# Optimization experiments

Measured on AMD Instinct MI355X. Metric: run time of the kernel, lower is better.

## Reference

```python
import jax, jax.numpy as jnp
import numpy as np

EPS = 1e-5
AVG_D_LOG = 2.302585092994046  # avg_d['log'] = log(10)

N, D, F, FE = 65536, 16, 64, 16
POST_IN = (4 * 3 + 1) * F  # (n_agg*n_scalers + 1) * in_dim = 832


def setup_inputs() -> dict:
    key = jax.random.key(0)
    ks = jax.random.split(key, 8)
    h = jax.random.normal(ks[0], (N, F), dtype=jnp.float32)
    edge_attr = jax.random.normal(ks[1], (N, D, FE), dtype=jnp.float32)
    nbr_idx = jax.random.randint(ks[2], (N, D), 0, N)
    pre_in = 2 * F + FE
    W_pre = jax.random.normal(ks[3], (pre_in, F), dtype=jnp.float32) / np.sqrt(pre_in)
    b_pre = jnp.zeros((F,), dtype=jnp.float32)
    W_post1 = jax.random.normal(ks[4], (POST_IN, F), dtype=jnp.float32) / np.sqrt(POST_IN)
    b_post1 = jnp.zeros((F,), dtype=jnp.float32)
    W_post2 = jax.random.normal(ks[5], (F, F), dtype=jnp.float32) / np.sqrt(F)
    b_post2 = jnp.zeros((F,), dtype=jnp.float32)
    return {"h": h, "edge_attr": edge_attr, "nbr_idx": nbr_idx,
            "W_pre": W_pre, "b_pre": b_pre,
            "W_post1": W_post1, "b_post1": b_post1,
            "W_post2": W_post2, "b_post2": b_post2}


def reference(h, edge_attr, nbr_idx, W_pre, b_pre, W_post1, b_post1, W_post2, b_post2):
    # pretrans: message MLP on cat([src_feat, dst_feat, edge_attr])
    h_src = h[nbr_idx]                                   # [N, D, F]
    h_dst = jnp.broadcast_to(h[:, None, :], h_src.shape)  # [N, D, F]
    z = jnp.concatenate([h_src, h_dst, edge_attr], axis=-1)  # [N, D, 2F+FE]
    e = jax.nn.relu(jnp.einsum('ndi,io->ndo', z, W_pre) + b_pre)  # [N, D, F]

    # multi-aggregator neighbor reduction (dim=-2)
    mean = jnp.mean(e, axis=-2)
    mx = jnp.max(e, axis=-2)
    mn = jnp.min(e, axis=-2)
    var = jax.nn.relu(jnp.mean(e * e, axis=-2) - mean * mean)
    std = jnp.sqrt(var + EPS)
    agg = jnp.concatenate([mean, mx, mn, std], axis=-1)  # [N, 4F]

    # degree scalers (fixed in-degree D)
    logD = jnp.asarray(np.log(D + 1.0), dtype=h.dtype)
    amp = agg * (logD / AVG_D_LOG)
    att = agg * (AVG_D_LOG / logD)
    agg = jnp.concatenate([agg, amp, att], axis=-1)      # [N, 12F]

    # posttrans MLP on cat([h, aggregated]) with residual (in_dim == out_dim)
    x = jnp.concatenate([h, agg], axis=-1)               # [N, 13F]
    x = jax.nn.relu(x @ W_post1 + b_post1)
    x = x @ W_post2 + b_post2
    return x + h
```

## Files before the change

### kernel.cpp

```cpp
#include <hip/hip_runtime.h>
#include <hip/hip_bf16.h>
#include <math.h>


#define N_NODES 65536
#define NBLK (N_NODES / 16)
#define GRID_PREP (NBLK + 64)
#define ASTRIDE 348
#define YSTRIDE 76

typedef float f32x4 __attribute__((ext_vector_type(4)));
typedef float f32x16 __attribute__((ext_vector_type(16)));
typedef short s16x8 __attribute__((ext_vector_type(8)));
typedef unsigned short us4 __attribute__((ext_vector_type(4)));
typedef int i32x4 __attribute__((ext_vector_type(4)));

__device__ __forceinline__ unsigned short f2bf(float f) {
    union { float f; unsigned int u; } v; v.f = f;
    unsigned int r = v.u + 0x7fffu + ((v.u >> 16) & 1u);
    return (unsigned short)(r >> 16);
}
__device__ __forceinline__ unsigned short f2bfh(float f) {
    __hip_bfloat16 b = __float2bfloat16(f);
    union { __hip_bfloat16 b; unsigned short u; } v; v.b = b; return v.u;
}
__device__ __forceinline__ float bf2f(unsigned short u) {
    union { unsigned int u; float f; } v; v.u = ((unsigned int)u) << 16; return v.f;
}
__device__ __forceinline__ unsigned char enc_u8(float x) {
    int q = __float2int_rn(x * 16.f) + 128;
    q = q < 0 ? 0 : (q > 255 ? 255 : q);
    return (unsigned char)q;
}

__global__ __launch_bounds__(256) void k_prep(const float* __restrict__ h,
                                              const float* __restrict__ Wpre,
                                              const float* __restrict__ b_pre,
                                              const float* __restrict__ Wp1,
                                              const float* __restrict__ Wp2,
                                              unsigned char* __restrict__ u8,
                                              unsigned short* __restrict__ vbf,
                                              unsigned short* __restrict__ wfullT,
                                              unsigned short* __restrict__ w3T,
                                              unsigned short* __restrict__ wp2T,
                                              float c1, float c2) {
    int t = threadIdx.x;
    if (blockIdx.x >= NBLK) {
        int c = blockIdx.x - NBLK;
        for (int k = t; k < 320; k += 256) {
            float v;
            if (k < 64) v = Wp1[k * 64 + c];
            else {
                int kk = k - 64;
                v = Wp1[(64 + kk) * 64 + c] + c1 * Wp1[(320 + kk) * 64 + c]
                                            + c2 * Wp1[(576 + kk) * 64 + c];
            }
            wfullT[c * 320 + k] = f2bf(v);
        }
        if (t < 16)              w3T[c * 16 + t]         = f2bf(Wpre[(128 + t) * 64 + c]);
        if (t >= 64 && t < 128)  wp2T[c * 64 + (t - 64)] = f2bf(Wp2[(t - 64) * 64 + c]);
        return;
    }

    __shared__ unsigned short hl[16 * 68];
    int lane = t & 63;
    int wv = __builtin_amdgcn_readfirstlane(t) >> 6;
    int c = lane & 15, g = lane >> 4;
    int node0 = blockIdx.x * 16;
    {
        int r = t >> 4, q = t & 15;
        float4 hv = *((const float4*)(h + (size_t)node0 * 64) + t);
        us4 o;
        o.x = f2bfh(hv.x); o.y = f2bfh(hv.y); o.z = f2bfh(hv.z); o.w = f2bfh(hv.w);
        *(us4*)&hl[r * 68 + q * 4] = o;
    }
    s16x8 bf[2][2];
    int woff = (wv < 2) ? 0 : 64;
    #pragma unroll
    for (int i2 = 0; i2 < 2; ++i2) {
        int wcol = ((wv & 1) * 32) + i2 * 16 + c;
        #pragma unroll
        for (int ks = 0; ks < 2; ++ks) {
            #pragma unroll
            for (int j = 0; j < 8; ++j)
                bf[i2][ks][j] = (short)f2bfh(Wpre[(woff + ks * 32 + g * 8 + j) * 64 + wcol]);
        }
    }
    __syncthreads();
    f32x4 acc0 = {0.f, 0.f, 0.f, 0.f}, acc1 = {0.f, 0.f, 0.f, 0.f};
    #pragma unroll
    for (int ks = 0; ks < 2; ++ks) {
        s16x8 a = *(const s16x8*)&hl[c * 68 + ks * 32 + g * 8];
        acc0 = __builtin_amdgcn_mfma_f32_16x16x32_bf16(a, bf[0][ks], acc0, 0, 0, 0);
        acc1 = __builtin_amdgcn_mfma_f32_16x16x32_bf16(a, bf[1][ks], acc1, 0, 0, 0);
    }
    #pragma unroll
    for (int i2 = 0; i2 < 2; ++i2) {
        int dcol = ((wv & 1) * 32) + i2 * 16 + c;
        const f32x4& av = i2 ? acc1 : acc0;
        if (wv < 2) {
            float bp = b_pre[dcol];
            #pragma unroll
            for (int i = 0; i < 4; ++i) {
                int row = g * 4 + i;
                u8[(size_t)(node0 + row) * 64 + dcol] = enc_u8(av[i] + bp);
            }
        } else {
            #pragma unroll
            for (int i = 0; i < 4; ++i) {
                int row = g * 4 + i;
                vbf[(size_t)(node0 + row) * 64 + dcol] = f2bfh(av[i]);
            }
        }
    }
}

__global__ __launch_bounds__(256, 4) void k_main(
    const float* __restrict__ h,
    const float* __restrict__ edge_attr,
    const int* __restrict__ nbr_idx,
    const float* __restrict__ b_post1,
    const float* __restrict__ b_post2,
    const unsigned char* __restrict__ u8,
    const unsigned short* __restrict__ vbf,
    const unsigned short* __restrict__ wfullT,
    const unsigned short* __restrict__ w3T,
    const unsigned short* __restrict__ wp2T,
    float* __restrict__ out) {
    __shared__ i32x4 u_lds4[1024];
    __shared__ i32x4 v_lds4[128];
    __shared__ unsigned short A_lds[16 * ASTRIDE];
    __shared__ unsigned short y1_lds[16 * YSTRIDE];
    unsigned char* u_lds = (unsigned char*)u_lds4;
    unsigned short* v_lds = (unsigned short*)v_lds4;

    int t = threadIdx.x;
    int lane = t & 63;
    int wu2 = __builtin_amdgcn_readfirstlane(t) >> 6;
    int c = lane & 15;
    int g = lane >> 4;
    int l32 = lane & 31;
    int h2 = lane >> 5;
    int ct = wu2 & 1;
    int wr = wu2 >> 1;
    int colb = ct * 32 + l32;
    int col16 = wu2 * 16 + c;
    int node0 = blockIdx.x * 16;

    s16x8 w3b = *(const s16x8*)&w3T[colb * 16 + h2 * 8];
    float b1c = b_post1[col16];
    float b2c = b_post2[col16];

    const char* eb = (const char*)edge_attr
                   + ((size_t)node0 * 16 + wr * 32 + l32) * 64 + h2 * 32;
    float4 xa0 = *(const float4*)(eb);
    float4 xb0 = *(const float4*)(eb + 16);
    float4 xa1 = *(const float4*)(eb + 4096);
    float4 xb1 = *(const float4*)(eb + 4096 + 16);
    float4 xa2 = *(const float4*)(eb + 8192);
    float4 xb2 = *(const float4*)(eb + 8192 + 16);
    float4 xa3 = *(const float4*)(eb + 12288);
    float4 xb3 = *(const float4*)(eb + 12288 + 16);

    #pragma unroll
    for (int it = 0; it < 4; ++it) {
        int row = (t >> 2) + 64 * it;
        int chunk = t & 3;
        int j = nbr_idx[node0 * 16 + row];
        *(i32x4*)&u_lds[row * 64 + chunk * 16] =
            *(const i32x4*)(u8 + ((size_t)j << 6) + chunk * 16);
    }
    if (t < 128)
        v_lds4[t] = *((const i32x4*)((const char*)vbf + ((size_t)node0 << 7)) + t);
    {
        int r = t >> 4, q = t & 15;
        float4 hv = *((const float4*)(h + (size_t)node0 * 64) + t);
        us4 o;
        o.x = f2bfh(hv.x); o.y = f2bfh(hv.y); o.z = f2bfh(hv.z); o.w = f2bfh(hv.w);
        *(us4*)&A_lds[r * ASTRIDE + q * 4] = o;
    }
    __syncthreads();

#define TILEC(X0, X1, IT) {                                                    \
    int rt = wr + 2 * (IT);                                                    \
    s16x8 a;                                                                   \
    a[0] = (short)f2bfh(X0.x); a[1] = (short)f2bfh(X0.y);                      \
    a[2] = (short)f2bfh(X0.z); a[3] = (short)f2bfh(X0.w);                      \
    a[4] = (short)f2bfh(X1.x); a[5] = (short)f2bfh(X1.y);                      \
    a[6] = (short)f2bfh(X1.z); a[7] = (short)f2bfh(X1.w);                      \
    f32x16 acc = {};                                                           \
    acc = __builtin_amdgcn_mfma_f32_32x32x16_bf16(a, w3b, acc, 0, 0, 0);       \
    const unsigned char* ur = &u_lds[(rt * 32 + 4 * h2) * 64 + colb];          \
    float uf[16];                                                              \
    _Pragma("unroll")                                                          \
    for (int q = 0; q < 4; ++q) {                                              \
        uf[4 * q + 0] = (float)ur[(8 * q + 0) * 64];                           \
        uf[4 * q + 1] = (float)ur[(8 * q + 1) * 64];                           \
        uf[4 * q + 2] = (float)ur[(8 * q + 2) * 64];                           \
        uf[4 * q + 3] = (float)ur[(8 * q + 3) * 64];                           \
    }                                                                          \
    float vv0 = bf2f(v_lds[(2 * rt + 0) * 64 + colb]) - 8.f;                   \
    float vv1 = bf2f(v_lds[(2 * rt + 1) * 64 + colb]) - 8.f;                   \
    float e0  = fmaxf(fmaf(uf[0],  0.0625f, acc[0]  + vv0), 0.f);              \
    float e1  = fmaxf(fmaf(uf[1],  0.0625f, acc[1]  + vv0), 0.f);              \
    float e2  = fmaxf(fmaf(uf[2],  0.0625f, acc[2]  + vv0), 0.f);              \
    float e3  = fmaxf(fmaf(uf[3],  0.0625f, acc[3]  + vv0), 0.f);              \
    float e4  = fmaxf(fmaf(uf[4],  0.0625f, acc[4]  + vv0), 0.f);              \
    float e5  = fmaxf(fmaf(uf[5],  0.0625f, acc[5]  + vv0), 0.f);              \
    float e6  = fmaxf(fmaf(uf[6],  0.0625f, acc[6]  + vv0), 0.f);              \
    float e7  = fmaxf(fmaf(uf[7],  0.0625f, acc[7]  + vv0), 0.f);              \
    float e8  = fmaxf(fmaf(uf[8],  0.0625f, acc[8]  + vv1), 0.f);              \
    float e9  = fmaxf(fmaf(uf[9],  0.0625f, acc[9]  + vv1), 0.f);              \
    float e10 = fmaxf(fmaf(uf[10], 0.0625f, acc[10] + vv1), 0.f);              \
    float e11 = fmaxf(fmaf(uf[11], 0.0625f, acc[11] + vv1), 0.f);              \
    float e12 = fmaxf(fmaf(uf[12], 0.0625f, acc[12] + vv1), 0.f);              \
    float e13 = fmaxf(fmaf(uf[13], 0.0625f, acc[13] + vv1), 0.f);              \
    float e14 = fmaxf(fmaf(uf[14], 0.0625f, acc[14] + vv1), 0.f);              \
    float e15 = fmaxf(fmaf(uf[15], 0.0625f, acc[15] + vv1), 0.f);              \
    float s1a = ((e0 + e1) + (e2 + e3)) + ((e4 + e5) + (e6 + e7));             \
    float s2a = fmaf(e0, e0, fmaf(e1, e1, fmaf(e2, e2, e3 * e3)))              \
              + fmaf(e4, e4, fmaf(e5, e5, fmaf(e6, e6, e7 * e7)));             \
    float mxa = fmaxf(fmaxf(fmaxf(e0, e1), fmaxf(e2, e3)),                     \
                      fmaxf(fmaxf(e4, e5), fmaxf(e6, e7)));                    \
    float mna = fminf(fminf(fminf(e0, e1), fminf(e2, e3)),                     \
                      fminf(fminf(e4, e5), fminf(e6, e7)));                    \
    float s1b = ((e8 + e9) + (e10 + e11)) + ((e12 + e13) + (e14 + e15));       \
    float s2b = fmaf(e8, e8, fmaf(e9, e9, fmaf(e10, e10, e11 * e11)))          \
              + fmaf(e12, e12, fmaf(e13, e13, fmaf(e14, e14, e15 * e15)));     \
    float mxb = fmaxf(fmaxf(fmaxf(e8, e9), fmaxf(e10, e11)),                   \
                      fmaxf(fmaxf(e12, e13), fmaxf(e14, e15)));                \
    float mnb = fminf(fminf(fminf(e8, e9), fminf(e10, e11)),                   \
                      fminf(fminf(e12, e13), fminf(e14, e15)));                \
    s1a += __shfl_xor(s1a, 32); s2a += __shfl_xor(s2a, 32);                    \
    mxa = fmaxf(mxa, __shfl_xor(mxa, 32)); mna = fminf(mna, __shfl_xor(mna, 32)); \
    s1b += __shfl_xor(s1b, 32); s2b += __shfl_xor(s2b, 32);                    \
    mxb = fmaxf(mxb, __shfl_xor(mxb, 32)); mnb = fminf(mnb, __shfl_xor(mnb, 32)); \
    float S1 = h2 ? s1b : s1a;                                                 \
    float S2 = h2 ? s2b : s2a;                                                 \
    float MX = h2 ? mxb : mxa;                                                 \
    float MN = h2 ? mnb : mna;                                                 \
    float M  = S1 * 0.0625f;                                                   \
    float SD = sqrtf(fmaxf(fmaf(-M, M, S2 * 0.0625f), 0.f) + 1e-5f);           \
    unsigned short* pd = &A_lds[(2 * rt + h2) * ASTRIDE + 64 + colb];          \
    pd[0]   = f2bfh(M);                                                        \
    pd[64]  = f2bfh(MX);                                                       \
    pd[128] = f2bfh(MN);                                                       \
    pd[192] = f2bfh(SD);                                                       \
}

    TILEC(xa0, xb0, 0)
    TILEC(xa1, xb1, 1)
    TILEC(xa2, xb2, 2)
    TILEC(xa3, xb3, 3)
#undef TILEC

    s16x8 wf[10];
    #pragma unroll
    for (int ks = 0; ks < 10; ++ks)
        wf[ks] = *(const s16x8*)&wfullT[col16 * 320 + ks * 32 + g * 8];
    __syncthreads();

    {
        f32x4 y1 = {0.f, 0.f, 0.f, 0.f};
        #pragma unroll
        for (int ks = 0; ks < 10; ++ks) {
            s16x8 a = *(const s16x8*)&A_lds[c * ASTRIDE + ks * 32 + g * 8];
            y1 = __builtin_amdgcn_mfma_f32_16x16x32_bf16(a, wf[ks], y1, 0, 0, 0);
        }
        #pragma unroll
        for (int i = 0; i < 4; ++i)
            y1_lds[(g * 4 + i) * YSTRIDE + col16] = f2bfh(fmaxf(y1[i] + b1c, 0.f));
    }

    s16x8 wp0 = *(const s16x8*)&wp2T[col16 * 64 + 0 * 32 + g * 8];
    s16x8 wp1 = *(const s16x8*)&wp2T[col16 * 64 + 1 * 32 + g * 8];
    __syncthreads();

    {
        f32x4 o = {0.f, 0.f, 0.f, 0.f};
        s16x8 a0 = *(const s16x8*)&y1_lds[c * YSTRIDE + 0 * 32 + g * 8];
        s16x8 a1 = *(const s16x8*)&y1_lds[c * YSTRIDE + 1 * 32 + g * 8];
        o = __builtin_amdgcn_mfma_f32_16x16x32_bf16(a0, wp0, o, 0, 0, 0);
        o = __builtin_amdgcn_mfma_f32_16x16x32_bf16(a1, wp1, o, 0, 0, 0);
        #pragma unroll
        for (int i = 0; i < 4; ++i) {
            int r = g * 4 + i;
            out[(size_t)(node0 + r) * 64 + col16] =
                o[i] + b2c + h[(size_t)(node0 + r) * 64 + col16];
        }
    }
}

extern "C" void kernel_launch(void* const* d_in, const int* in_sizes, int n_in,
                              void* d_out, int out_size, void* d_ws, size_t ws_size,
                              hipStream_t stream) {
    const float* h         = (const float*)d_in[0];
    const float* edge_attr = (const float*)d_in[1];
    const int*   nbr_idx   = (const int*)d_in[2];
    const float* W_pre     = (const float*)d_in[3];
    const float* b_pre     = (const float*)d_in[4];
    const float* W_post1   = (const float*)d_in[5];
    const float* b_post1   = (const float*)d_in[6];
    const float* W_post2   = (const float*)d_in[7];
    const float* b_post2   = (const float*)d_in[8];
    float* out = (float*)d_out;

    size_t need = (size_t)N_NODES * 64
                + (size_t)N_NODES * 64 * 2
                + (64 * 320 + 64 * 16 + 64 * 64) * 2;
    if (ws_size < need) return;
    unsigned char*  u8p    = (unsigned char*)d_ws;
    unsigned short* vbf    = (unsigned short*)(u8p + (size_t)N_NODES * 64);
    unsigned short* wfullT = vbf + (size_t)N_NODES * 64;
    unsigned short* w3T    = wfullT + 64 * 320;
    unsigned short* wp2T   = w3T + 64 * 16;

    double ld = log(16.0 + 1.0);
    const double AVG = 2.302585092994046;
    float c1 = (float)(ld / AVG);
    float c2 = (float)(AVG / ld);

    k_prep<<<GRID_PREP, 256, 0, stream>>>(h, W_pre, b_pre, W_post1, W_post2,
                                          u8p, vbf, wfullT, w3T, wp2T, c1, c2);
    k_main<<<NBLK, 256, 0, stream>>>(h, edge_attr, nbr_idx, b_post1, b_post2,
                                     u8p, vbf, wfullT, w3T, wp2T, out);
}
```

Baseline: 62.28 us.

## Make k_main persistent over four node groups with double-buffered prefetch

Each block now processes four consecutive 16-node groups instead of one, cutting the grid by four. While one group is computed, the next group's neighbour gathers, v rows, edge_attr and h are prefetched into registers and written into double-buffered LDS, and neighbour indices are fetched two groups ahead. The aim is to hide gather and global-load latency behind the MFMA and reduction work. In exchange the kernel uses more registers and LDS (launch bounds drop to 3), and with only 1024 blocks there is less parallelism across the GPU.

```diff
diff --git a/kernel.cpp b/kernel.cpp
--- a/kernel.cpp
+++ b/kernel.cpp
@@ -5,6 +5,8 @@
 
 #define N_NODES 65536
 #define NBLK (N_NODES / 16)
+#define NITER 4
+#define GRID_MAIN (NBLK / NITER)
 #define GRID_PREP (NBLK + 64)
 #define ASTRIDE 348
 #define YSTRIDE 76
@@ -115,7 +117,7 @@
     }
 }
 
-__global__ __launch_bounds__(256, 4) void k_main(
+__global__ __launch_bounds__(256, 3) void k_main(
     const float* __restrict__ h,
     const float* __restrict__ edge_attr,
     const int* __restrict__ nbr_idx,
@@ -127,12 +129,10 @@
     const unsigned short* __restrict__ w3T,
     const unsigned short* __restrict__ wp2T,
     float* __restrict__ out) {
-    __shared__ i32x4 u_lds4[1024];
-    __shared__ i32x4 v_lds4[128];
+    __shared__ unsigned char  u_lds[2][16384];
+    __shared__ unsigned short v_lds[2][1024];
     __shared__ unsigned short A_lds[16 * ASTRIDE];
     __shared__ unsigned short y1_lds[16 * YSTRIDE];
-    unsigned char* u_lds = (unsigned char*)u_lds4;
-    unsigned short* v_lds = (unsigned short*)v_lds4;
 
     int t = threadIdx.x;
     int lane = t & 63;
@@ -145,52 +145,91 @@
     int wr = wu2 >> 1;
     int colb = ct * 32 + l32;
     int col16 = wu2 * 16 + c;
-    int node0 = blockIdx.x * 16;
+    int ch = t & 3;
+    int srow = t >> 2;
 
     s16x8 w3b = *(const s16x8*)&w3T[colb * 16 + h2 * 8];
     float b1c = b_post1[col16];
     float b2c = b_post2[col16];
 
-    const char* eb = (const char*)edge_attr
-                   + ((size_t)node0 * 16 + wr * 32 + l32) * 64 + h2 * 32;
-    float4 xa0 = *(const float4*)(eb);
-    float4 xb0 = *(const float4*)(eb + 16);
-    float4 xa1 = *(const float4*)(eb + 4096);
-    float4 xb1 = *(const float4*)(eb + 4096 + 16);
-    float4 xa2 = *(const float4*)(eb + 8192);
-    float4 xb2 = *(const float4*)(eb + 8192 + 16);
-    float4 xa3 = *(const float4*)(eb + 12288);
-    float4 xb3 = *(const float4*)(eb + 12288 + 16);
-
-    #pragma unroll
-    for (int it = 0; it < 4; ++it) {
-        int row = (t >> 2) + 64 * it;
-        int chunk = t & 3;
-        int j = nbr_idx[node0 * 16 + row];
-        *(i32x4*)&u_lds[row * 64 + chunk * 16] =
-            *(const i32x4*)(u8 + ((size_t)j << 6) + chunk * 16);
-    }
-    if (t < 128)
-        v_lds4[t] = *((const i32x4*)((const char*)vbf + ((size_t)node0 << 7)) + t);
+    int grp0 = blockIdx.x * NITER;
+    float4 xaC[4], xbC[4], xaN[4], xbN[4];
+    int jc[4], jn[4];
+
     {
-        int r = t >> 4, q = t & 15;
-        float4 hv = *((const float4*)(h + (size_t)node0 * 64) + t);
-        us4 o;
-        o.x = f2bfh(hv.x); o.y = f2bfh(hv.y); o.z = f2bfh(hv.z); o.w = f2bfh(hv.w);
-        *(us4*)&A_lds[r * ASTRIDE + q * 4] = o;
+        const int* nb = nbr_idx + (size_t)grp0 * 256;
+        i32x4 s[4];
+        #pragma unroll
+        for (int i = 0; i < 4; ++i) {
+            int j = nb[srow + 64 * i];
+            s[i] = *(const i32x4*)(u8 + ((size_t)j << 6) + ch * 16);
+        }
+        i32x4 sv = {};
+        if (t < 128)
+            sv = *(const i32x4*)((const char*)vbf + (size_t)grp0 * 2048 + t * 16);
+        const char* eb = (const char*)edge_attr
+                       + ((size_t)grp0 * 256 + wr * 32 + l32) * 64 + h2 * 32;
+        #pragma unroll
+        for (int k = 0; k < 4; ++k) {
+            xaC[k] = *(const float4*)(eb + k * 4096);
+            xbC[k] = *(const float4*)(eb + k * 4096 + 16);
+        }
+        float4 hv = *((const float4*)(h + (size_t)grp0 * 1024) + t);
+        #pragma unroll
+        for (int i = 0; i < 4; ++i)
+            jc[i] = nbr_idx[(size_t)(grp0 + 1) * 256 + srow + 64 * i];
+        #pragma unroll
+        for (int i = 0; i < 4; ++i)
+            *(i32x4*)&u_lds[0][i * 4096 + t * 16] = s[i];
+        if (t < 128) *(i32x4*)&v_lds[0][t * 8] = sv;
+        {
+            int r = t >> 4, q = t & 15;
+            us4 o;
+            o.x = f2bfh(hv.x); o.y = f2bfh(hv.y); o.z = f2bfh(hv.z); o.w = f2bfh(hv.w);
+            *(us4*)&A_lds[r * ASTRIDE + q * 4] = o;
+        }
     }
     __syncthreads();
 
-#define TILEC(X0, X1, IT) {                                                    \
+    int b = 0;
+    for (int it = 0; it < NITER; ++it) {
+        int grp = grp0 + it;
+        size_t node0 = (size_t)grp * 16;
+        bool pf = (it + 1 < NITER);
+        int grpn = grp + 1;
+
+        i32x4 su[4]; i32x4 sv = {}; float4 hn = {0.f, 0.f, 0.f, 0.f};
+        if (pf) {
+            #pragma unroll
+            for (int i = 0; i < 4; ++i)
+                su[i] = *(const i32x4*)(u8 + ((size_t)jc[i] << 6) + ch * 16);
+            if (t < 128)
+                sv = *(const i32x4*)((const char*)vbf + (size_t)grpn * 2048 + t * 16);
+            const char* ebn = (const char*)edge_attr
+                            + ((size_t)grpn * 256 + wr * 32 + l32) * 64 + h2 * 32;
+            #pragma unroll
+            for (int k = 0; k < 4; ++k) {
+                xaN[k] = *(const float4*)(ebn + k * 4096);
+                xbN[k] = *(const float4*)(ebn + k * 4096 + 16);
+            }
+            hn = *((const float4*)(h + (size_t)grpn * 1024) + t);
+            if (it + 2 < NITER) {
+                #pragma unroll
+                for (int i = 0; i < 4; ++i)
+                    jn[i] = nbr_idx[(size_t)(grp + 2) * 256 + srow + 64 * i];
+            }
+        }
+
+#define TILEC(IT) {                                                            \
     int rt = wr + 2 * (IT);                                                    \
     s16x8 a;                                                                   \
-    a[0] = (short)f2bfh(X0.x); a[1] = (short)f2bfh(X0.y);                      \
-    a[2] = (short)f2bfh(X0.z); a[3] = (short)f2bfh(X0.w);                      \
-    a[4] = (short)f2bfh(X1.x); a[5] = (short)f2bfh(X1.y);                      \
-    a[6] = (short)f2bfh(X1.z); a[7] = (short)f2bfh(X1.w);                      \
+    a[0] = (short)f2bfh(xaC[IT].x); a[1] = (short)f2bfh(xaC[IT].y);            \
+    a[2] = (short)f2bfh(xaC[IT].z); a[3] = (short)f2bfh(xaC[IT].w);            \
+    a[4] = (short)f2bfh(xbC[IT].x); a[5] = (short)f2bfh(xbC[IT].y);            \
+    a[6] = (short)f2bfh(xbC[IT].z); a[7] = (short)f2bfh(xbC[IT].w);            \
     f32x16 acc = {};                                                           \
     acc = __builtin_amdgcn_mfma_f32_32x32x16_bf16(a, w3b, acc, 0, 0, 0);       \
-    const unsigned char* ur = &u_lds[(rt * 32 + 4 * h2) * 64 + colb];          \
+    const unsigned char* ur = &u_lds[b][(rt * 32 + 4 * h2) * 64 + colb];       \
     float uf[16];                                                              \
     _Pragma("unroll")                                                          \
     for (int q = 0; q < 4; ++q) {                                              \
@@ -199,8 +238,8 @@
         uf[4 * q + 2] = (float)ur[(8 * q + 2) * 64];                           \
         uf[4 * q + 3] = (float)ur[(8 * q + 3) * 64];                           \
     }                                                                          \
-    float vv0 = bf2f(v_lds[(2 * rt + 0) * 64 + colb]) - 8.f;                   \
-    float vv1 = bf2f(v_lds[(2 * rt + 1) * 64 + colb]) - 8.f;                   \
+    float vv0 = bf2f(v_lds[b][(2 * rt + 0) * 64 + colb]) - 8.f;                \
+    float vv1 = bf2f(v_lds[b][(2 * rt + 1) * 64 + colb]) - 8.f;                \
     float e0  = fmaxf(fmaf(uf[0],  0.0625f, acc[0]  + vv0), 0.f);              \
     float e1  = fmaxf(fmaf(uf[1],  0.0625f, acc[1]  + vv0), 0.f);              \
     float e2  = fmaxf(fmaf(uf[2],  0.0625f, acc[2]  + vv0), 0.f);              \
@@ -247,46 +286,67 @@
     pd[128] = f2bfh(MN);                                                       \
     pd[192] = f2bfh(SD);                                                       \
 }
-
-    TILEC(xa0, xb0, 0)
-    TILEC(xa1, xb1, 1)
-    TILEC(xa2, xb2, 2)
-    TILEC(xa3, xb3, 3)
+        TILEC(0)
+        TILEC(1)
+        TILEC(2)
+        TILEC(3)
 #undef TILEC
 
-    s16x8 wf[10];
-    #pragma unroll
-    for (int ks = 0; ks < 10; ++ks)
-        wf[ks] = *(const s16x8*)&wfullT[col16 * 320 + ks * 32 + g * 8];
-    __syncthreads();
-
-    {
-        f32x4 y1 = {0.f, 0.f, 0.f, 0.f};
-        #pragma unroll
-        for (int ks = 0; ks < 10; ++ks) {
-            s16x8 a = *(const s16x8*)&A_lds[c * ASTRIDE + ks * 32 + g * 8];
-            y1 = __builtin_amdgcn_mfma_f32_16x16x32_bf16(a, wf[ks], y1, 0, 0, 0);
-        }
-        #pragma unroll
-        for (int i = 0; i < 4; ++i)
-            y1_lds[(g * 4 + i) * YSTRIDE + col16] = f2bfh(fmaxf(y1[i] + b1c, 0.f));
-    }
-
-    s16x8 wp0 = *(const s16x8*)&wp2T[col16 * 64 + 0 * 32 + g * 8];
-    s16x8 wp1 = *(const s16x8*)&wp2T[col16 * 64 + 1 * 32 + g * 8];
-    __syncthreads();
-
-    {
-        f32x4 o = {0.f, 0.f, 0.f, 0.f};
-        s16x8 a0 = *(const s16x8*)&y1_lds[c * YSTRIDE + 0 * 32 + g * 8];
-        s16x8 a1 = *(const s16x8*)&y1_lds[c * YSTRIDE + 1 * 32 + g * 8];
-        o = __builtin_amdgcn_mfma_f32_16x16x32_bf16(a0, wp0, o, 0, 0, 0);
-        o = __builtin_amdgcn_mfma_f32_16x16x32_bf16(a1, wp1, o, 0, 0, 0);
-        #pragma unroll
-        for (int i = 0; i < 4; ++i) {
-            int r = g * 4 + i;
-            out[(size_t)(node0 + r) * 64 + col16] =
-                o[i] + b2c + h[(size_t)(node0 + r) * 64 + col16];
+        if (pf) {
+            #pragma unroll
+            for (int i = 0; i < 4; ++i)
+                *(i32x4*)&u_lds[b ^ 1][i * 4096 + t * 16] = su[i];
+            if (t < 128) *(i32x4*)&v_lds[b ^ 1][t * 8] = sv;
+        }
+
+        s16x8 wf[10];
+        #pragma unroll
+        for (int ks = 0; ks < 10; ++ks)
+            wf[ks] = *(const s16x8*)&wfullT[col16 * 320 + ks * 32 + g * 8];
+        __syncthreads();
+
+        {
+            f32x4 y1 = {0.f, 0.f, 0.f, 0.f};
+            #pragma unroll
+            for (int ks = 0; ks < 10; ++ks) {
+                s16x8 a = *(const s16x8*)&A_lds[c * ASTRIDE + ks * 32 + g * 8];
+                y1 = __builtin_amdgcn_mfma_f32_16x16x32_bf16(a, wf[ks], y1, 0, 0, 0);
+            }
+            #pragma unroll
+            for (int i = 0; i < 4; ++i)
+                y1_lds[(g * 4 + i) * YSTRIDE + col16] = f2bfh(fmaxf(y1[i] + b1c, 0.f));
+        }
+        s16x8 wp0 = *(const s16x8*)&wp2T[col16 * 64 + 0 * 32 + g * 8];
+        s16x8 wp1 = *(const s16x8*)&wp2T[col16 * 64 + 1 * 32 + g * 8];
+        __syncthreads();
+
+        if (pf) {
+            int r = t >> 4, q = t & 15;
+            us4 o;
+            o.x = f2bfh(hn.x); o.y = f2bfh(hn.y); o.z = f2bfh(hn.z); o.w = f2bfh(hn.w);
+            *(us4*)&A_lds[r * ASTRIDE + q * 4] = o;
+        }
+
+        {
+            f32x4 o = {0.f, 0.f, 0.f, 0.f};
+            s16x8 a0 = *(const s16x8*)&y1_lds[c * YSTRIDE + 0 * 32 + g * 8];
+            s16x8 a1 = *(const s16x8*)&y1_lds[c * YSTRIDE + 1 * 32 + g * 8];
+            o = __builtin_amdgcn_mfma_f32_16x16x32_bf16(a0, wp0, o, 0, 0, 0);
+            o = __builtin_amdgcn_mfma_f32_16x16x32_bf16(a1, wp1, o, 0, 0, 0);
+            #pragma unroll
+            for (int i = 0; i < 4; ++i) {
+                int r = g * 4 + i;
+                out[(node0 + r) * 64 + col16] =
+                    o[i] + b2c + h[(node0 + r) * 64 + col16];
+            }
+        }
+
+        if (pf) {
+            #pragma unroll
+            for (int k = 0; k < 4; ++k) { xaC[k] = xaN[k]; xbC[k] = xbN[k]; }
+            #pragma unroll
+            for (int i = 0; i < 4; ++i) jc[i] = jn[i];
+            b ^= 1;
         }
     }
 }
@@ -322,6 +382,6 @@
 
     k_prep<<<GRID_PREP, 256, 0, stream>>>(h, W_pre, b_pre, W_post1, W_post2,
                                           u8p, vbf, wfullT, w3T, wp2T, c1, c2);
-    k_main<<<NBLK, 256, 0, stream>>>(h, edge_attr, nbr_idx, b_post1, b_post2,
-                                     u8p, vbf, wfullT, w3T, wp2T, out);
-}
+    k_main<<<GRID_MAIN, 256, 0, stream>>>(h, edge_attr, nbr_idx, b_post1, b_post2,
+                                          u8p, vbf, wfullT, w3T, wp2T, out);
+}
```

New measurement: 116.2 us. 86.6% more time.
